# Kernel tuning notes

Hardware: AMD Instinct MI355X
Metric: run time of the kernel (lower is better)

The kernel has to match this reference:

```python
import jax, jax.numpy as jnp
import numpy as np

B = 32768
N_INT = 32          # num_intruders
OWN_D = 3
INT_D = 7
ATTN_D = 128
HID = 256
OUT_D = 2
OBS_D = OWN_D + N_INT * INT_D  # 227
NEG_SLOPE = 0.2

def _lrelu(x):
    return jax.nn.leaky_relu(x, NEG_SLOPE)

def setup_inputs() -> dict:
    key = jax.random.key(0)
    ks = jax.random.split(key, 16)
    obs = jax.random.normal(ks[0], (B, OBS_D), dtype=jnp.float32)
    pad = jax.random.bernoulli(ks[1], 0.25, (B, N_INT))
    intr = obs[:, OWN_D:].reshape(B, N_INT, INT_D)
    intr = jnp.where(pad[:, :, None], 0.0, intr)
    obs = jnp.concatenate([obs[:, :OWN_D], intr.reshape(B, -1)], axis=1)
    def glorot(k, shape):
        fan_in, fan_out = shape[0], shape[-1]
        lim = jnp.sqrt(6.0 / (fan_in + fan_out))
        return jax.random.uniform(k, shape, jnp.float32, -lim, lim)
    return {
        "obs": obs,
        "own_W": glorot(ks[2], (OWN_D, ATTN_D)), "own_b": jnp.zeros((ATTN_D,), jnp.float32),
        "int_W": glorot(ks[3], (INT_D, ATTN_D)), "int_b": jnp.zeros((ATTN_D,), jnp.float32),
        "Wq": glorot(ks[4], (ATTN_D, ATTN_D)),
        "Wk": glorot(ks[5], (ATTN_D, ATTN_D)),
        "Wv": glorot(ks[6], (ATTN_D, ATTN_D)),
        "v_att": glorot(ks[7], (ATTN_D, 1))[:, 0],
        "proj_W": glorot(ks[8], (ATTN_D, ATTN_D)), "proj_b": jnp.zeros((ATTN_D,), jnp.float32),
        "h1_W": glorot(ks[9], (2 * ATTN_D, HID)), "h1_b": jnp.zeros((HID,), jnp.float32),
        "h2_W": glorot(ks[10], (HID, HID)), "h2_b": jnp.zeros((HID,), jnp.float32),
        "out_W": glorot(ks[11], (HID, OUT_D)), "out_b": jnp.zeros((OUT_D,), jnp.float32),
    }

def reference(obs, own_W, own_b, int_W, int_b, Wq, Wk, Wv, v_att,
              proj_W, proj_b, h1_W, h1_b, h2_W, h2_b, out_W, out_b):
    own = obs[:, :OWN_D]                                   # [B,3]
    intr = obs[:, OWN_D:OWN_D + N_INT * INT_D].reshape(-1, N_INT, INT_D)  # [B,N,7]
    own_e = _lrelu(own @ own_W + own_b)                    # [B,128]
    int_e = _lrelu(intr @ int_W + int_b)                   # [B,N,128]
    q = own_e @ Wq                                         # [B,128]
    k = int_e @ Wk                                         # [B,N,128]
    v = int_e @ Wv                                         # [B,N,128]
    energy = jnp.tanh(q[:, None, :] + k)                   # [B,N,128]
    scores = energy @ v_att                                # [B,N]
    is_padding = jnp.abs(intr).sum(axis=2) < 1e-6          # [B,N]
    scores = jnp.where(is_padding, -jnp.inf, scores)
    alpha = jax.nn.softmax(scores, axis=-1)
    alpha = jnp.nan_to_num(alpha, nan=0.0)
    ctx = jnp.einsum('bn,bnd->bd', alpha, v)               # [B,128]
    attn_vec = jnp.tanh(ctx @ proj_W + proj_b)             # [B,128]
    x = jnp.concatenate([own_e, attn_vec], axis=1)         # [B,256]
    x = _lrelu(x @ h1_W + h1_b)
    x = _lrelu(x @ h2_W + h2_b)
    return x @ out_W + out_b                               # [B,2]
```

## Files before the change

kernel.cpp:

```cpp
#include <hip/hip_runtime.h>
#include <hip/hip_bf16.h>
#include <math.h>

typedef _Float16 half2_t __attribute__((ext_vector_type(2)));
typedef _Float16 f16x8   __attribute__((ext_vector_type(8)));
typedef float    f32x4   __attribute__((ext_vector_type(4)));

constexpr int BATCH = 32768;
constexpr int NI   = 32;
constexpr int OWND = 3;
constexpr int INTD = 7;
constexpr int AD   = 128;
constexpr int HIDN = 256;
constexpr int OUTD = 2;
constexpr int OBSD = OWND + NI * INTD;
constexpr int IEPITCH = 68;
constexpr float C2L2E = 2.885390081777927f;

__device__ __forceinline__ half2_t u2h(unsigned u) { return __builtin_bit_cast(half2_t, u); }
__device__ __forceinline__ unsigned packf(float a, float b) {
    half2_t h = { (_Float16)a, (_Float16)b };
    return __builtin_bit_cast(unsigned, h);
}
__device__ __forceinline__ float lrelu(float x) { return fmaxf(x, 0.2f * x); }
__device__ __forceinline__ float exp2fast(float x) { return __builtin_amdgcn_exp2f(x); }
__device__ __forceinline__ float fast_tanh(float x) {
    float e = exp2fast(x * C2L2E);
    return 1.0f - 2.0f * __builtin_amdgcn_rcpf(e + 1.0f);
}

constexpr int UW_PWKQ = 0;
constexpr int UW_PWVF = 16384;
constexpr int UW_PPRF = 24576;
constexpr int UW_PIWF = 32768;
constexpr int UW_PH1F = 34816;
constexpr int UW_PH2F = 67584;
constexpr int UW_FULL = 100352;
constexpr size_t XBUF_U = (size_t)BATCH * (HIDN / 2);

__global__ __launch_bounds__(256) void pack_full(
    const float* __restrict__ Wq, const float* __restrict__ Wk,
    const float* __restrict__ Wv, const float* __restrict__ Pr,
    const float* __restrict__ IW, const float* __restrict__ IB,
    const float* __restrict__ H1, const float* __restrict__ H2,
    unsigned* __restrict__ dst)
{
    int u = blockIdx.x * 256 + threadIdx.x;
    if (u >= UW_FULL) return;
    if (u < 16384) {
        int f = u >> 8, kt = f >> 3, nt = f & 7;
        int idx = u & 255, lane = idx >> 2, w = idx & 3;
        int qd = lane >> 4, lo = lane & 15;
        const float* src = (kt < 4) ? Wk : Wq;
        int ktp = kt & 3;
        int r0 = 32 * ktp + 8 * qd + 2 * w, col = 16 * nt + lo;
        dst[u] = packf(src[r0 * 128 + col], src[(r0 + 1) * 128 + col]);
    } else if (u < 32768) {
        const float* src = (u < 24576) ? Wv : Pr;
        int i = (u - 16384) & 8191;
        int f = i >> 8, kt = f >> 3, nt = f & 7;
        int idx = i & 255, lane = idx >> 2, w = idx & 3;
        int qd = lane >> 4, lo = lane & 15;
        int r0 = 32 * kt + 8 * qd + 2 * w, col = 16 * nt + lo;
        dst[u] = packf(src[r0 * 128 + col], src[(r0 + 1) * 128 + col]);
    } else if (u < 34816) {
        int i = u - 32768;
        int nt = i >> 8;
        int idx = i & 255, lane = idx >> 2, w = idx & 3;
        int qd = lane >> 4, lo = lane & 15;
        int r0 = 8 * qd + 2 * w, col = 16 * nt + lo;
        float v0 = (r0 < INTD) ? IW[r0 * 128 + col] : 0.f;
        float v1 = (r0 + 1 < INTD) ? IW[(r0 + 1) * 128 + col]
                 : ((r0 + 1 == INTD) ? IB[col] : 0.f);
        dst[u] = packf(v0, v1);
    } else {
        int i = u - 34816;
        const float* src = (i < 32768) ? H1 : H2;
        i &= 32767;
        int f = i >> 8, nt = f >> 3, kt = f & 7;
        int idx = i & 255, lane = idx >> 2, w = idx & 3;
        int qd = lane >> 4, lo = lane & 15;
        int r0 = 32 * kt + 8 * qd + 2 * w, col = 16 * nt + lo;
        dst[u] = packf(src[r0 * 256 + col], src[(r0 + 1) * 256 + col]);
    }
}

__global__ __launch_bounds__(256) void qgemm(
    const float* __restrict__ obs, const float* __restrict__ own_W,
    const float* __restrict__ own_b, const unsigned* __restrict__ pWkqF,
    float* __restrict__ qall)
{
    const int wv = threadIdx.x >> 6;
    const int l  = threadIdx.x & 63;
    const int lo = l & 15, qd = l >> 4;
    const size_t row0 = (size_t)blockIdx.x * 64 + (size_t)wv * 16;

    __shared__ __align__(16) float    s_own[4][16][4];
    __shared__ __align__(16) unsigned s_oe[4][16 * 68];

    if (l < 16) {
        const float* orow = obs + (row0 + l) * OBSD;
        s_own[wv][l][0] = orow[0]; s_own[wv][l][1] = orow[1]; s_own[wv][l][2] = orow[2];
    }

    {
        const float x0 = s_own[wv][lo][0], x1 = s_own[wv][lo][1], x2 = s_own[wv][lo][2];
        #pragma unroll
        for (int jj = 0; jj < 8; jj++) {
            const int c4 = qd * 32 + jj * 4;
            float4 wb = *(const float4*)(own_b + c4);
            float4 w0 = *(const float4*)(own_W + 0 * AD + c4);
            float4 w1 = *(const float4*)(own_W + 1 * AD + c4);
            float4 w2 = *(const float4*)(own_W + 2 * AD + c4);
            float v0 = lrelu(wb.x + x0 * w0.x + x1 * w1.x + x2 * w2.x);
            float v1 = lrelu(wb.y + x0 * w0.y + x1 * w1.y + x2 * w2.y);
            float v2 = lrelu(wb.z + x0 * w0.z + x1 * w1.z + x2 * w2.z);
            float v3 = lrelu(wb.w + x0 * w0.w + x1 * w1.w + x2 * w2.w);
            s_oe[wv][lo * 68 + (c4 >> 1)]     = packf(v0, v1);
            s_oe[wv][lo * 68 + (c4 >> 1) + 1] = packf(v2, v3);
        }
    }

    f16x8 aE[4];
    #pragma unroll
    for (int kt = 0; kt < 4; kt++) {
        uint4 au = *(const uint4*)(&s_oe[wv][lo * 68 + 16 * kt + 4 * qd]);
        aE[kt] = __builtin_bit_cast(f16x8, au);
    }
    #pragma unroll
    for (int nt = 0; nt < 8; nt++) {
        f32x4 acc = {0.f, 0.f, 0.f, 0.f};
        #pragma unroll
        for (int kt = 0; kt < 4; kt++) {
            uint4 bu = *(const uint4*)(pWkqF + (((kt + 4) * 8 + nt) << 8) + (l << 2));
            acc = __builtin_amdgcn_mfma_f32_16x16x32_f16(aE[kt], __builtin_bit_cast(f16x8, bu), acc, 0, 0, 0);
        }
        #pragma unroll
        for (int r = 0; r < 4; r++)
            qall[(row0 + 4 * qd + r) * AD + 16 * nt + lo] = acc[r];
    }
}

__global__ __launch_bounds__(256) void attn(
    const float* __restrict__ obs,
    const float* __restrict__ own_W, const float* __restrict__ own_b,
    const unsigned* __restrict__ pIWF, const float* __restrict__ int_b,
    const unsigned* __restrict__ pWkqF, const float* __restrict__ v_att,
    const float* __restrict__ qall,
    unsigned* __restrict__ xbuf)
{
    const int wv = threadIdx.x >> 6;
    const int l  = threadIdx.x & 63;
    const int b  = blockIdx.x * 4 + wv;
    const int d0 = 2 * l;
    const int lo = l & 15, qd = l >> 4;
    const bool useQ = (qall != nullptr);

    __shared__ __align__(16) float    s_obs[4][OBSD];
    __shared__ __align__(16) unsigned s_ieb[4][NI * IEPITCH];
    __shared__ __align__(16) unsigned s_ownh[4][AD / 2];
    __shared__ __align__(16) float    s_sc[4][NI];

    const float* orow = obs + (size_t)b * OBSD;
    for (int i = l; i < OBSD; i += 64) s_obs[wv][i] = orow[i];

    float oe0 = own_b[d0], oe1 = own_b[d0 + 1];
    #pragma unroll
    for (int j = 0; j < OWND; j++) {
        float x = s_obs[wv][j];
        oe0 += x * own_W[j * AD + d0];
        oe1 += x * own_W[j * AD + d0 + 1];
    }
    oe0 = lrelu(oe0); oe1 = lrelu(oe1);
    s_ownh[wv][l] = packf(oe0, oe1);

    int padf = 0;
    if (l < NI) {
        float su = 0.f;
        #pragma unroll
        for (int j = 0; j < INTD; j++) su += fabsf(s_obs[wv][OWND + l * INTD + j]);
        padf = (su < 1e-6f);
    }

    float qe[8];
    if (useQ) {
        const float* qrow = qall + (size_t)b * AD;
        #pragma unroll
        for (int nt = 0; nt < 8; nt++) qe[nt] = qrow[16 * nt + lo] * C2L2E;
    } else {
        #pragma unroll
        for (int nt = 0; nt < 8; nt++) qe[nt] = 0.f;
    }

    f16x8 aInt[2];
    #pragma unroll
    for (int t = 0; t < 2; t++) {
        #pragma unroll
        for (int j = 0; j < 8; j++) {
            int k = 8 * qd + j;
            float v;
            if (k < INTD)       v = s_obs[wv][OWND + (16 * t + lo) * INTD + k];
            else if (k == INTD) v = 1.0f;
            else                v = 0.f;
            aInt[t][j] = (_Float16)v;
        }
    }
    _Float16* s_ieh = (_Float16*)s_ieb[wv];
    #pragma unroll
    for (int nt = 0; nt < 8; nt++) {
        uint4 bu = *(const uint4*)(pIWF + (nt << 8) + (l << 2));
        f16x8 bf = __builtin_bit_cast(f16x8, bu);
        f32x4 z = {0.f, 0.f, 0.f, 0.f};
        f32x4 c0 = __builtin_amdgcn_mfma_f32_16x16x32_f16(aInt[0], bf, z, 0, 0, 0);
        f32x4 c1 = __builtin_amdgcn_mfma_f32_16x16x32_f16(aInt[1], bf, z, 0, 0, 0);
        const int cswz = (16 * nt + lo) ^ (qd << 3);
        #pragma unroll
        for (int r = 0; r < 4; r++) {
            s_ieh[(4 * qd + r) * 136 + cswz]      = (_Float16)lrelu(c0[r]);
            s_ieh[(16 + 4 * qd + r) * 136 + cswz] = (_Float16)lrelu(c1[r]);
        }
    }

    const int slo = ((lo >> 2) & 3) << 2;
    f16x8 aIE[2][4];
    #pragma unroll
    for (int t = 0; t < 2; t++)
        #pragma unroll
        for (int kt = 0; kt < 4; kt++) {
            uint4 au = *(const uint4*)(&s_ieb[wv][(16 * t + lo) * IEPITCH + ((16 * kt + 4 * qd) ^ slo)]);
            aIE[t][kt] = __builtin_bit_cast(f16x8, au);
        }

    float sA0[4] = {0.f, 0.f, 0.f, 0.f};
    float sA1[4] = {0.f, 0.f, 0.f, 0.f};
    float vsum = 0.f;
    #pragma unroll
    for (int nt = 0; nt < 8; nt++) {
        f32x4 acc0 = {0.f, 0.f, 0.f, 0.f};
        f32x4 acc1 = {0.f, 0.f, 0.f, 0.f};
        if (useQ) {
            #pragma unroll
            for (int kt = 0; kt < 4; kt++) {
                uint4 bu = *(const uint4*)(pWkqF + ((kt * 8 + nt) << 8) + (l << 2));
                f16x8 bf = __builtin_bit_cast(f16x8, bu);
                acc0 = __builtin_amdgcn_mfma_f32_16x16x32_f16(aIE[0][kt], bf, acc0, 0, 0, 0);
                acc1 = __builtin_amdgcn_mfma_f32_16x16x32_f16(aIE[1][kt], bf, acc1, 0, 0, 0);
            }
        } else {
            #pragma unroll
            for (int kt = 0; kt < 8; kt++) {
                uint4 bu = *(const uint4*)(pWkqF + ((kt * 8 + nt) << 8) + (l << 2));
                f16x8 bf = __builtin_bit_cast(f16x8, bu);
                f16x8 af0, af1;
                if (kt < 4) { af0 = aIE[0][kt]; af1 = aIE[1][kt]; }
                else {
                    uint4 au = *(const uint4*)(&s_ownh[wv][16 * (kt - 4) + 4 * qd]);
                    af0 = __builtin_bit_cast(f16x8, au);
                    af1 = af0;
                }
                acc0 = __builtin_amdgcn_mfma_f32_16x16x32_f16(af0, bf, acc0, 0, 0, 0);
                acc1 = __builtin_amdgcn_mfma_f32_16x16x32_f16(af1, bf, acc1, 0, 0, 0);
            }
        }
        const float vc   = v_att[16 * nt + lo];
        const float n2vc = -2.0f * vc;
        vsum += vc;
        #pragma unroll
        for (int r = 0; r < 4; r++) {
            float t0 = exp2fast(fmaf(acc0[r], C2L2E, qe[nt]));
            sA0[r] = fmaf(n2vc, __builtin_amdgcn_rcpf(t0 + 1.0f), sA0[r]);
            float t1 = exp2fast(fmaf(acc1[r], C2L2E, qe[nt]));
            sA1[r] = fmaf(n2vc, __builtin_amdgcn_rcpf(t1 + 1.0f), sA1[r]);
        }
    }
    #pragma unroll
    for (int r = 0; r < 4; r++) { sA0[r] += vsum; sA1[r] += vsum; }
    #pragma unroll
    for (int r = 0; r < 4; r++) {
        #pragma unroll
        for (int w = 1; w <= 8; w <<= 1) {
            sA0[r] += __shfl_xor(sA0[r], w, 64);
            sA1[r] += __shfl_xor(sA1[r], w, 64);
        }
    }
    if (lo == 0) {
        #pragma unroll
        for (int r = 0; r < 4; r++) {
            s_sc[wv][4 * qd + r]      = sA0[r];
            s_sc[wv][16 + 4 * qd + r] = sA1[r];
        }
    }

    {
        float sval = -INFINITY;
        if (l < NI && !padf) sval = s_sc[wv][l];
        float mm = sval;
        #pragma unroll
        for (int w = 1; w <= 16; w <<= 1) mm = fmaxf(mm, __shfl_xor(mm, w, 64));
        float e = (sval > -INFINITY) ? __expf(sval - mm) : 0.f;
        float dd = e;
        #pragma unroll
        for (int w = 1; w <= 16; w <<= 1) dd += __shfl_xor(dd, w, 64);
        if (l < NI) s_sc[wv][l] = (dd > 0.f) ? e * __builtin_amdgcn_rcpf(dd) : 0.f;
    }

    float sv0 = 0.f, sv1 = 0.f;
    #pragma unroll
    for (int n = 0; n < NI; n++) {
        const int sn = ((n >> 2) & 3) << 2;
        half2_t ie = u2h(s_ieb[wv][n * IEPITCH + (l ^ sn)]);
        float a = s_sc[wv][n];
        sv0 += a * (float)ie.x; sv1 += a * (float)ie.y;
    }
    xbuf[(size_t)b * (HIDN / 2) + l]      = s_ownh[wv][l];
    xbuf[(size_t)b * (HIDN / 2) + 64 + l] = packf(sv0, sv1);
}

__global__ __launch_bounds__(512) void mlp8w(
    const unsigned* __restrict__ xbuf,
    const unsigned* __restrict__ pWvF, const float* __restrict__ proj_b,
    const unsigned* __restrict__ pPrF,
    const unsigned* __restrict__ pH1F, const float* __restrict__ h1_b,
    const unsigned* __restrict__ pH2F, const float* __restrict__ h2_b,
    const float* __restrict__ out_W,   const float* __restrict__ out_b,
    float* __restrict__ res)
{
    const int tid = threadIdx.x;
    const int wv  = tid >> 6;
    const int l   = tid & 63;
    const int lo  = l & 15, qd = l >> 4;
    const size_t row0 = (size_t)blockIdx.x * 32;

    __shared__ __align__(16) unsigned s_x[32 * 132];
    __shared__ __align__(16) unsigned s_scr[32 * 68];
    __shared__ __align__(16) float    s_red[8][32][2];

    #pragma unroll
    for (int it = 0; it < 2; it++) {
        int i = tid + it * 512;
        int r = i >> 5, cq = i & 31;
        uint4 u = *(const uint4*)(xbuf + (row0 + r) * 128 + cq * 4);
        if (cq < 16) *(uint4*)(&s_x[r * 132 + cq * 4]) = u;
        else         *(uint4*)(&s_scr[r * 68 + (cq - 16) * 4]) = u;
    }
    __syncthreads();

    _Float16* s_ctxh = (_Float16*)s_scr;
    _Float16* s_xh   = (_Float16*)s_x;

    #pragma unroll
    for (int rowg = 0; rowg < 2; rowg++) {
        const int rb = 16 * rowg;
        f16x8 aS[4];
        #pragma unroll
        for (int kt = 0; kt < 4; kt++) {
            uint4 au = *(const uint4*)(&s_scr[(rb + lo) * 68 + 16 * kt + 4 * qd]);
            aS[kt] = __builtin_bit_cast(f16x8, au);
        }
        __syncthreads();
        {
            const int nt = wv;
            f32x4 acc = {0.f, 0.f, 0.f, 0.f};
            #pragma unroll
            for (int kt = 0; kt < 4; kt++) {
                uint4 bu = *(const uint4*)(pWvF + ((kt * 8 + nt) << 8) + (l << 2));
                acc = __builtin_amdgcn_mfma_f32_16x16x32_f16(aS[kt], __builtin_bit_cast(f16x8, bu), acc, 0, 0, 0);
            }
            #pragma unroll
            for (int r = 0; r < 4; r++)
                s_ctxh[(rb + 4 * qd + r) * 136 + 16 * nt + lo] = (_Float16)acc[r];
        }
    }
    __syncthreads();

    #pragma unroll
    for (int rowg = 0; rowg < 2; rowg++) {
        const int rb = 16 * rowg;
        f16x8 aC[4];
        #pragma unroll
        for (int kt = 0; kt < 4; kt++) {
            uint4 au = *(const uint4*)(&s_scr[(rb + lo) * 68 + 16 * kt + 4 * qd]);
            aC[kt] = __builtin_bit_cast(f16x8, au);
        }
        {
            const int nt = wv;
            f32x4 acc = {0.f, 0.f, 0.f, 0.f};
            #pragma unroll
            for (int kt = 0; kt < 4; kt++) {
                uint4 bu = *(const uint4*)(pPrF + ((kt * 8 + nt) << 8) + (l << 2));
                acc = __builtin_amdgcn_mfma_f32_16x16x32_f16(aC[kt], __builtin_bit_cast(f16x8, bu), acc, 0, 0, 0);
            }
            const float bn = proj_b[16 * nt + lo];
            #pragma unroll
            for (int r = 0; r < 4; r++)
                s_xh[(rb + 4 * qd + r) * 264 + 128 + 16 * nt + lo] = (_Float16)fast_tanh(acc[r] + bn);
        }
    }
    __syncthreads();

    {
        f16x8 aX[8];
        #pragma unroll
        for (int kt = 0; kt < 8; kt++) {
            uint4 au = *(const uint4*)(&s_x[lo * 132 + 16 * kt + 4 * qd]);
            aX[kt] = __builtin_bit_cast(f16x8, au);
        }
        __syncthreads();
        #pragma unroll
        for (int ni = 0; ni < 2; ni++) {
            const int nt = 2 * wv + ni;
            f32x4 acc = {0.f, 0.f, 0.f, 0.f};
            #pragma unroll
            for (int kt = 0; kt < 8; kt++) {
                uint4 bu = *(const uint4*)(pH1F + ((nt * 8 + kt) << 8) + (l << 2));
                acc = __builtin_amdgcn_mfma_f32_16x16x32_f16(aX[kt], __builtin_bit_cast(f16x8, bu), acc, 0, 0, 0);
            }
            const float bn = h1_b[16 * nt + lo];
            #pragma unroll
            for (int r = 0; r < 4; r++)
                s_xh[(4 * qd + r) * 264 + 16 * nt + lo] = (_Float16)lrelu(acc[r] + bn);
        }
        #pragma unroll
        for (int kt = 0; kt < 8; kt++) {
            uint4 au = *(const uint4*)(&s_x[(16 + lo) * 132 + 16 * kt + 4 * qd]);
            aX[kt] = __builtin_bit_cast(f16x8, au);
        }
        __syncthreads();
        #pragma unroll
        for (int ni = 0; ni < 2; ni++) {
            const int nt = 2 * wv + ni;
            f32x4 acc = {0.f, 0.f, 0.f, 0.f};
            #pragma unroll
            for (int kt = 0; kt < 8; kt++) {
                uint4 bu = *(const uint4*)(pH1F + ((nt * 8 + kt) << 8) + (l << 2));
                acc = __builtin_amdgcn_mfma_f32_16x16x32_f16(aX[kt], __builtin_bit_cast(f16x8, bu), acc, 0, 0, 0);
            }
            const float bn = h1_b[16 * nt + lo];
            #pragma unroll
            for (int r = 0; r < 4; r++)
                s_xh[(16 + 4 * qd + r) * 264 + 16 * nt + lo] = (_Float16)lrelu(acc[r] + bn);
        }
    }
    __syncthreads();

    #pragma unroll
    for (int rowg = 0; rowg < 2; rowg++) {
        const int rb = 16 * rowg;
        f16x8 aH[8];
        #pragma unroll
        for (int kt = 0; kt < 8; kt++) {
            uint4 au = *(const uint4*)(&s_x[(rb + lo) * 132 + 16 * kt + 4 * qd]);
            aH[kt] = __builtin_bit_cast(f16x8, au);
        }
        float o0[4] = {0.f, 0.f, 0.f, 0.f};
        float o1[4] = {0.f, 0.f, 0.f, 0.f};
        #pragma unroll
        for (int ni = 0; ni < 2; ni++) {
            const int nt = 2 * wv + ni;
            f32x4 acc = {0.f, 0.f, 0.f, 0.f};
            #pragma unroll
            for (int kt = 0; kt < 8; kt++) {
                uint4 bu = *(const uint4*)(pH2F + ((nt * 8 + kt) << 8) + (l << 2));
                acc = __builtin_amdgcn_mfma_f32_16x16x32_f16(aH[kt], __builtin_bit_cast(f16x8, bu), acc, 0, 0, 0);
            }
            const float bn = h2_b[16 * nt + lo];
            float2 w = *(const float2*)(out_W + (size_t)(16 * nt + lo) * OUTD);
            #pragma unroll
            for (int r = 0; r < 4; r++) {
                float v = lrelu(acc[r] + bn);
                o0[r] += v * w.x; o1[r] += v * w.y;
            }
        }
        #pragma unroll
        for (int r = 0; r < 4; r++) {
            #pragma unroll
            for (int w = 1; w <= 8; w <<= 1) {
                o0[r] += __shfl_xor(o0[r], w, 64);
                o1[r] += __shfl_xor(o1[r], w, 64);
            }
        }
        if (lo == 0) {
            #pragma unroll
            for (int r = 0; r < 4; r++) {
                s_red[wv][rb + 4 * qd + r][0] = o0[r];
                s_red[wv][rb + 4 * qd + r][1] = o1[r];
            }
        }
    }
    __syncthreads();
    if (tid < 64) {
        int r = tid >> 1, cmp = tid & 1;
        float s = out_b[cmp];
        #pragma unroll
        for (int w = 0; w < 8; w++) s += s_red[w][r][cmp];
        res[(row0 + r) * OUTD + cmp] = s;
    }
}

__global__ __launch_bounds__(256) void copy_out(const float* __restrict__ src,
                                               float* __restrict__ dst, int n4) {
    int i = blockIdx.x * 256 + threadIdx.x;
    if (i < n4) ((float4*)dst)[i] = ((const float4*)src)[i];
}

extern "C" void kernel_launch(void* const* d_in, const int* in_sizes, int n_in,
                              void* d_out, int out_size, void* d_ws, size_t ws_size,
                              hipStream_t stream) {
    const float* obs    = (const float*)d_in[0];
    const float* own_W  = (const float*)d_in[1];
    const float* own_b  = (const float*)d_in[2];
    const float* int_W  = (const float*)d_in[3];
    const float* int_b  = (const float*)d_in[4];
    const float* Wq     = (const float*)d_in[5];
    const float* Wk     = (const float*)d_in[6];
    const float* Wv     = (const float*)d_in[7];
    const float* v_att  = (const float*)d_in[8];
    const float* proj_W = (const float*)d_in[9];
    const float* proj_b = (const float*)d_in[10];
    const float* h1_W   = (const float*)d_in[11];
    const float* h1_b   = (const float*)d_in[12];
    const float* h2_W   = (const float*)d_in[13];
    const float* h2_b   = (const float*)d_in[14];
    const float* out_W  = (const float*)d_in[15];
    const float* out_b  = (const float*)d_in[16];

    const size_t res_bytes  = (size_t)BATCH * OUTD * sizeof(float);
    const size_t q_bytes    = (size_t)BATCH * AD * sizeof(float);
    const size_t base_bytes = (size_t)UW_FULL * 4 + XBUF_U * 4 + res_bytes;
    const int n4 = BATCH * OUTD / 4;

    if (ws_size >= base_bytes + q_bytes) {
        unsigned* pw   = (unsigned*)d_ws;
        unsigned* xbuf = pw + UW_FULL;
        float*    qall = (float*)(xbuf + XBUF_U);
        float*    res  = qall + (size_t)BATCH * AD;
        pack_full<<<(UW_FULL + 255) / 256, 256, 0, stream>>>(
            Wq, Wk, Wv, proj_W, int_W, int_b, h1_W, h2_W, pw);
        qgemm<<<BATCH / 64, 256, 0, stream>>>(obs, own_W, own_b, pw + UW_PWKQ, qall);
        attn<<<BATCH / 4, 256, 0, stream>>>(
            obs, own_W, own_b, pw + UW_PIWF, int_b,
            pw + UW_PWKQ, v_att, qall, xbuf);
        mlp8w<<<BATCH / 32, 512, 0, stream>>>(
            xbuf, pw + UW_PWVF, proj_b, pw + UW_PPRF,
            pw + UW_PH1F, h1_b, pw + UW_PH2F, h2_b, out_W, out_b, res);
        copy_out<<<(n4 + 255) / 256, 256, 0, stream>>>(res, (float*)d_out, n4);
    } else if (ws_size >= base_bytes) {
        unsigned* pw   = (unsigned*)d_ws;
        unsigned* xbuf = pw + UW_FULL;
        float*    res  = (float*)(xbuf + XBUF_U);
        pack_full<<<(UW_FULL + 255) / 256, 256, 0, stream>>>(
            Wq, Wk, Wv, proj_W, int_W, int_b, h1_W, h2_W, pw);
        attn<<<BATCH / 4, 256, 0, stream>>>(
            obs, own_W, own_b, pw + UW_PIWF, int_b,
            pw + UW_PWKQ, v_att, nullptr, xbuf);
        mlp8w<<<BATCH / 32, 512, 0, stream>>>(
            xbuf, pw + UW_PWVF, proj_b, pw + UW_PPRF,
            pw + UW_PH1F, h1_b, pw + UW_PH2F, h2_b, out_W, out_b, res);
        copy_out<<<(n4 + 255) / 256, 256, 0, stream>>>(res, (float*)d_out, n4);
    }
}
```

Before: 238.6 us.

## Fuse query GEMM into attention kernel via block-shared MFMA

Removes the separate qgemm kernel and its global q buffer. Inside the attention kernel, the four waves of a block together compute q for the block's four rows with MFMA: each wave handles two of the eight output column tiles and writes them to shared memory, reusing the s_obs region. This removes one launch and the global write and read of a B×128 float q array. The cost is two block-wide barriers, and a redundant MFMA in which only 4 of 16 A rows are useful.

```diff
diff --git a/kernel.cpp b/kernel.cpp
--- a/kernel.cpp
+++ b/kernel.cpp
@@ -85,68 +85,11 @@
     }
 }
 
-__global__ __launch_bounds__(256) void qgemm(
-    const float* __restrict__ obs, const float* __restrict__ own_W,
-    const float* __restrict__ own_b, const unsigned* __restrict__ pWkqF,
-    float* __restrict__ qall)
-{
-    const int wv = threadIdx.x >> 6;
-    const int l  = threadIdx.x & 63;
-    const int lo = l & 15, qd = l >> 4;
-    const size_t row0 = (size_t)blockIdx.x * 64 + (size_t)wv * 16;
-
-    __shared__ __align__(16) float    s_own[4][16][4];
-    __shared__ __align__(16) unsigned s_oe[4][16 * 68];
-
-    if (l < 16) {
-        const float* orow = obs + (row0 + l) * OBSD;
-        s_own[wv][l][0] = orow[0]; s_own[wv][l][1] = orow[1]; s_own[wv][l][2] = orow[2];
-    }
-
-    {
-        const float x0 = s_own[wv][lo][0], x1 = s_own[wv][lo][1], x2 = s_own[wv][lo][2];
-        #pragma unroll
-        for (int jj = 0; jj < 8; jj++) {
-            const int c4 = qd * 32 + jj * 4;
-            float4 wb = *(const float4*)(own_b + c4);
-            float4 w0 = *(const float4*)(own_W + 0 * AD + c4);
-            float4 w1 = *(const float4*)(own_W + 1 * AD + c4);
-            float4 w2 = *(const float4*)(own_W + 2 * AD + c4);
-            float v0 = lrelu(wb.x + x0 * w0.x + x1 * w1.x + x2 * w2.x);
-            float v1 = lrelu(wb.y + x0 * w0.y + x1 * w1.y + x2 * w2.y);
-            float v2 = lrelu(wb.z + x0 * w0.z + x1 * w1.z + x2 * w2.z);
-            float v3 = lrelu(wb.w + x0 * w0.w + x1 * w1.w + x2 * w2.w);
-            s_oe[wv][lo * 68 + (c4 >> 1)]     = packf(v0, v1);
-            s_oe[wv][lo * 68 + (c4 >> 1) + 1] = packf(v2, v3);
-        }
-    }
-
-    f16x8 aE[4];
-    #pragma unroll
-    for (int kt = 0; kt < 4; kt++) {
-        uint4 au = *(const uint4*)(&s_oe[wv][lo * 68 + 16 * kt + 4 * qd]);
-        aE[kt] = __builtin_bit_cast(f16x8, au);
-    }
-    #pragma unroll
-    for (int nt = 0; nt < 8; nt++) {
-        f32x4 acc = {0.f, 0.f, 0.f, 0.f};
-        #pragma unroll
-        for (int kt = 0; kt < 4; kt++) {
-            uint4 bu = *(const uint4*)(pWkqF + (((kt + 4) * 8 + nt) << 8) + (l << 2));
-            acc = __builtin_amdgcn_mfma_f32_16x16x32_f16(aE[kt], __builtin_bit_cast(f16x8, bu), acc, 0, 0, 0);
-        }
-        #pragma unroll
-        for (int r = 0; r < 4; r++)
-            qall[(row0 + 4 * qd + r) * AD + 16 * nt + lo] = acc[r];
-    }
-}
-
 __global__ __launch_bounds__(256) void attn(
     const float* __restrict__ obs,
     const float* __restrict__ own_W, const float* __restrict__ own_b,
-    const unsigned* __restrict__ pIWF, const float* __restrict__ int_b,
+    const unsigned* __restrict__ pIWF,
     const unsigned* __restrict__ pWkqF, const float* __restrict__ v_att,
-    const float* __restrict__ qall,
     unsigned* __restrict__ xbuf)
 {
     const int wv = threadIdx.x >> 6;
@@ -154,7 +97,6 @@
     const int b  = blockIdx.x * 4 + wv;
     const int d0 = 2 * l;
     const int lo = l & 15, qd = l >> 4;
-    const bool useQ = (qall != nullptr);
 
     __shared__ __align__(16) float    s_obs[4][OBSD];
     __shared__ __align__(16) unsigned s_ieb[4][NI * IEPITCH];
@@ -180,16 +122,6 @@
         #pragma unroll
         for (int j = 0; j < INTD; j++) su += fabsf(s_obs[wv][OWND + l * INTD + j]);
         padf = (su < 1e-6f);
-    }
-
-    float qe[8];
-    if (useQ) {
-        const float* qrow = qall + (size_t)b * AD;
-        #pragma unroll
-        for (int nt = 0; nt < 8; nt++) qe[nt] = qrow[16 * nt + lo] * C2L2E;
-    } else {
-        #pragma unroll
-        for (int nt = 0; nt < 8; nt++) qe[nt] = 0.f;
     }
 
     f16x8 aInt[2];
@@ -205,6 +137,38 @@
             aInt[t][j] = (_Float16)v;
         }
     }
+
+    __syncthreads();
+
+    float* s_q = (float*)s_obs;
+    {
+        f16x8 aQ[4];
+        #pragma unroll
+        for (int kt = 0; kt < 4; kt++) {
+            uint4 au = *(const uint4*)(&s_ownh[lo & 3][16 * kt + 4 * qd]);
+            aQ[kt] = __builtin_bit_cast(f16x8, au);
+        }
+        #pragma unroll
+        for (int ni = 0; ni < 2; ni++) {
+            const int nt = 2 * wv + ni;
+            f32x4 acc = {0.f, 0.f, 0.f, 0.f};
+            #pragma unroll
+            for (int kt = 0; kt < 4; kt++) {
+                uint4 bu = *(const uint4*)(pWkqF + (((kt + 4) * 8 + nt) << 8) + (l << 2));
+                acc = __builtin_amdgcn_mfma_f32_16x16x32_f16(aQ[kt], __builtin_bit_cast(f16x8, bu), acc, 0, 0, 0);
+            }
+            if (qd == 0) {
+                #pragma unroll
+                for (int r = 0; r < 4; r++) s_q[r * AD + 16 * nt + lo] = acc[r];
+            }
+        }
+    }
+    __syncthreads();
+
+    float qe[8];
+    #pragma unroll
+    for (int nt = 0; nt < 8; nt++) qe[nt] = s_q[wv * AD + 16 * nt + lo] * C2L2E;
+
     _Float16* s_ieh = (_Float16*)s_ieb[wv];
     #pragma unroll
     for (int nt = 0; nt < 8; nt++) {
@@ -238,29 +202,12 @@
     for (int nt = 0; nt < 8; nt++) {
         f32x4 acc0 = {0.f, 0.f, 0.f, 0.f};
         f32x4 acc1 = {0.f, 0.f, 0.f, 0.f};
-        if (useQ) {
-            #pragma unroll
-            for (int kt = 0; kt < 4; kt++) {
-                uint4 bu = *(const uint4*)(pWkqF + ((kt * 8 + nt) << 8) + (l << 2));
-                f16x8 bf = __builtin_bit_cast(f16x8, bu);
-                acc0 = __builtin_amdgcn_mfma_f32_16x16x32_f16(aIE[0][kt], bf, acc0, 0, 0, 0);
-                acc1 = __builtin_amdgcn_mfma_f32_16x16x32_f16(aIE[1][kt], bf, acc1, 0, 0, 0);
-            }
-        } else {
-            #pragma unroll
-            for (int kt = 0; kt < 8; kt++) {
-                uint4 bu = *(const uint4*)(pWkqF + ((kt * 8 + nt) << 8) + (l << 2));
-                f16x8 bf = __builtin_bit_cast(f16x8, bu);
-                f16x8 af0, af1;
-                if (kt < 4) { af0 = aIE[0][kt]; af1 = aIE[1][kt]; }
-                else {
-                    uint4 au = *(const uint4*)(&s_ownh[wv][16 * (kt - 4) + 4 * qd]);
-                    af0 = __builtin_bit_cast(f16x8, au);
-                    af1 = af0;
-                }
-                acc0 = __builtin_amdgcn_mfma_f32_16x16x32_f16(af0, bf, acc0, 0, 0, 0);
-                acc1 = __builtin_amdgcn_mfma_f32_16x16x32_f16(af1, bf, acc1, 0, 0, 0);
-            }
+        #pragma unroll
+        for (int kt = 0; kt < 4; kt++) {
+            uint4 bu = *(const uint4*)(pWkqF + ((kt * 8 + nt) << 8) + (l << 2));
+            f16x8 bf = __builtin_bit_cast(f16x8, bu);
+            acc0 = __builtin_amdgcn_mfma_f32_16x16x32_f16(aIE[0][kt], bf, acc0, 0, 0, 0);
+            acc1 = __builtin_amdgcn_mfma_f32_16x16x32_f16(aIE[1][kt], bf, acc1, 0, 0, 0);
         }
         const float vc   = v_att[16 * nt + lo];
         const float n2vc = -2.0f * vc;
@@ -525,34 +472,18 @@
     const float* out_b  = (const float*)d_in[16];
 
     const size_t res_bytes  = (size_t)BATCH * OUTD * sizeof(float);
-    const size_t q_bytes    = (size_t)BATCH * AD * sizeof(float);
     const size_t base_bytes = (size_t)UW_FULL * 4 + XBUF_U * 4 + res_bytes;
     const int n4 = BATCH * OUTD / 4;
 
-    if (ws_size >= base_bytes + q_bytes) {
-        unsigned* pw   = (unsigned*)d_ws;
-        unsigned* xbuf = pw + UW_FULL;
-        float*    qall = (float*)(xbuf + XBUF_U);
-        float*    res  = qall + (size_t)BATCH * AD;
-        pack_full<<<(UW_FULL + 255) / 256, 256, 0, stream>>>(
-            Wq, Wk, Wv, proj_W, int_W, int_b, h1_W, h2_W, pw);
-        qgemm<<<BATCH / 64, 256, 0, stream>>>(obs, own_W, own_b, pw + UW_PWKQ, qall);
-        attn<<<BATCH / 4, 256, 0, stream>>>(
-            obs, own_W, own_b, pw + UW_PIWF, int_b,
-            pw + UW_PWKQ, v_att, qall, xbuf);
-        mlp8w<<<BATCH / 32, 512, 0, stream>>>(
-            xbuf, pw + UW_PWVF, proj_b, pw + UW_PPRF,
-            pw + UW_PH1F, h1_b, pw + UW_PH2F, h2_b, out_W, out_b, res);
-        copy_out<<<(n4 + 255) / 256, 256, 0, stream>>>(res, (float*)d_out, n4);
-    } else if (ws_size >= base_bytes) {
+    if (ws_size >= base_bytes) {
         unsigned* pw   = (unsigned*)d_ws;
         unsigned* xbuf = pw + UW_FULL;
         float*    res  = (float*)(xbuf + XBUF_U);
         pack_full<<<(UW_FULL + 255) / 256, 256, 0, stream>>>(
             Wq, Wk, Wv, proj_W, int_W, int_b, h1_W, h2_W, pw);
         attn<<<BATCH / 4, 256, 0, stream>>>(
-            obs, own_W, own_b, pw + UW_PIWF, int_b,
-            pw + UW_PWKQ, v_att, nullptr, xbuf);
+            obs, own_W, own_b, pw + UW_PIWF,
+            pw + UW_PWKQ, v_att, xbuf);
         mlp8w<<<BATCH / 32, 512, 0, stream>>>(
             xbuf, pw + UW_PWVF, proj_b, pw + UW_PPRF,
             pw + UW_PH1F, h1_b, pw + UW_PH2F, h2_b, out_W, out_b, res);
```

Measured after the change: 240.2 us. About the same (+0.7%).
